# Kernel tuning notes

Hardware: AMD Instinct MI355X
Metric: run time of the kernel (lower is better)

Reference implementation:

```python
import jax, jax.numpy as jnp
import numpy as np

N_DRUG, N_CELL, N_GENE = 1000, 1000, 6000
N = N_DRUG + N_CELL + N_GENE
H1, H2, H3, HEADS = 256, 128, 128, 4
E = 160000
B = 10000


def _gat_layer(x, src, dst, ea, W, b, a_s, a_d, We, a_e, bias, heads, ch):
    # PyG GATConv (single shared lin for src/dst), edge_dim=1, concat=True, slope=0.2
    n = x.shape[0]
    xw = (x @ W + b).reshape(n, heads, ch)                     # [N,H,C]
    a_src = jnp.einsum('nhc,hc->nh', xw, a_s)                  # [N,H]
    a_dst = jnp.einsum('nhc,hc->nh', xw, a_d)
    eemb = (ea[:, None] @ We).reshape(-1, heads, ch)           # [E',H,C]
    a_edge = jnp.einsum('ehc,hc->eh', eemb, a_e)               # [E',H]
    alpha = jax.nn.leaky_relu(a_src[src] + a_dst[dst] + a_edge, 0.2)
    # segment softmax over destination node (flow source->target)
    m = jax.ops.segment_max(alpha, dst, num_segments=n)
    ex = jnp.exp(alpha - m[dst])
    denom = jax.ops.segment_sum(ex, dst, num_segments=n)
    att = ex / (denom[dst] + 1e-16)                            # [E',H]
    out = jax.ops.segment_sum(xw[src] * att[:, :, None], dst, num_segments=n)
    return out.reshape(n, heads * ch) + bias, att


def _graph_norm(x, gamma, beta, mean_scale, eps=1e-5):
    mu = x.mean(0)
    out = x - mean_scale * mu
    var = (out * out).mean(0)
    return gamma * out / jnp.sqrt(var + eps) + beta


def _attn_mat(src, dst, att, n):
    # original sets every edge entry to the scalar mean of all attention weights
    return jnp.zeros((n, n), dtype=att.dtype).at[src, dst].set(att.mean())


def setup_inputs() -> dict:
    key = jax.random.key(0)
    ks = jax.random.split(key, 40)
    s = 0.1
    inp = {
        'drug': jax.random.normal(ks[0], (N_DRUG, N_DRUG), jnp.float32),
        'cell': jax.random.normal(ks[1], (N_CELL, N_CELL), jnp.float32),
        'gene': jax.random.normal(ks[2], (N_GENE, N_GENE), jnp.float32),
        'edge_attr': jax.random.uniform(ks[3], (E,), jnp.float32),
        'edge_index': jax.random.randint(ks[4], (2, E), 0, N),
        'idx_drug': jax.random.randint(ks[5], (B,), 0, N_DRUG),
        'idx_cell': jax.random.randint(ks[6], (B,), 0, N),
        # type-specific input projections
        'W_drug': jax.random.normal(ks[7], (N_DRUG, H1)) * s, 'b_drug': jnp.zeros((H1,)),
        'W_cell': jax.random.normal(ks[8], (N_CELL, H1)) * s, 'b_cell': jnp.zeros((H1,)),
        'W_gene': jax.random.normal(ks[9], (N_GENE, H1)) * s, 'b_gene': jnp.zeros((H1,)),
        # gat1
        'W1': jax.random.normal(ks[10], (H1, HEADS * H2)) * s, 'b1': jnp.zeros((HEADS * H2,)),
        'att_src1': jax.random.normal(ks[11], (HEADS, H2)) * s,
        'att_dst1': jax.random.normal(ks[12], (HEADS, H2)) * s,
        'We1': jax.random.normal(ks[13], (1, HEADS * H2)) * s,
        'att_e1': jax.random.normal(ks[14], (HEADS, H2)) * s,
        'bias1': jnp.zeros((HEADS * H2,)),
        'g1': jnp.ones((HEADS * H2,)), 'be1': jnp.zeros((HEADS * H2,)), 'ms1': jnp.ones((HEADS * H2,)),
        # gat2
        'W2': jax.random.normal(ks[15], (HEADS * H2, HEADS * H3)) * s, 'b2': jnp.zeros((HEADS * H3,)),
        'att_src2': jax.random.normal(ks[16], (HEADS, H3)) * s,
        'att_dst2': jax.random.normal(ks[17], (HEADS, H3)) * s,
        'We2': jax.random.normal(ks[18], (1, HEADS * H3)) * s,
        'att_e2': jax.random.normal(ks[19], (HEADS, H3)) * s,
        'bias2': jnp.zeros((HEADS * H3,)),
        'g2': jnp.ones((HEADS * H3,)), 'be2': jnp.zeros((HEADS * H3,)), 'ms2': jnp.ones((HEADS * H3,)),
        # head
        'Wout': jax.random.normal(ks[20], (2 * HEADS * H3, 1)) * s, 'bout': jnp.zeros((1,)),
    }
    return inp


def reference(drug, cell, gene, edge_attr, edge_index, idx_drug, idx_cell,
              W_drug, b_drug, W_cell, b_cell, W_gene, b_gene,
              W1, b1, att_src1, att_dst1, We1, att_e1, bias1, g1, be1, ms1,
              W2, b2, att_src2, att_dst2, We2, att_e2, bias2, g2, be2, ms2,
              Wout, bout):
    x = jnp.concatenate([drug @ W_drug + b_drug,
                         cell @ W_cell + b_cell,
                         gene @ W_gene + b_gene], axis=0)       # [N,H1]
    # GATConv adds self-loops with edge_attr filled by the mean edge attribute
    loop = jnp.arange(N)
    src = jnp.concatenate([edge_index[0], loop])
    dst = jnp.concatenate([edge_index[1], loop])
    ea = jnp.concatenate([edge_attr, jnp.full((N,), edge_attr.mean(), edge_attr.dtype)])

    x, att1 = _gat_layer(x, src, dst, ea, W1, b1, att_src1, att_dst1, We1, att_e1, bias1, HEADS, H2)
    all_att = _attn_mat(src, dst, att1, N)
    x = jax.nn.relu(_graph_norm(x, g1, be1, ms1))               # dropout = identity (eval)

    x, att2 = _gat_layer(x, src, dst, ea, W2, b2, att_src2, att_dst2, We2, att_e2, bias2, HEADS, H3)
    all_att = all_att + _attn_mat(src, dst, att2, N)
    x = jax.nn.relu(_graph_norm(x, g2, be2, ms2))

    x = jnp.concatenate([x[idx_drug], x[idx_cell]], axis=1) @ Wout + bout  # [B,1]
    return x, all_att
```

## Files before the change

kernel.cpp:

```cpp
#include <hip/hip_runtime.h>
#include <math.h>

#define NDRUG 1000
#define NCELL 1000
#define NGENE 6000
#define NNODE 8000
#define H1 256
#define HD  512
#define E0  160000
#define ET  168000
#define BSZ 10000
#define GKP 6016
#define ZSPLIT 8
#define ZCH 768

typedef __attribute__((ext_vector_type(8))) short bf16x8;
typedef __attribute__((ext_vector_type(4))) float f32x4;

__device__ inline unsigned short f2bf(float f)
{
    unsigned u = __float_as_uint(f);
    u += 0x7fffu + ((u >> 16) & 1u);
    return (unsigned short)(u >> 16);
}
__device__ inline float bf2f(unsigned short h)
{
    return __uint_as_float(((unsigned)h) << 16);
}

__global__ void cvt_pad2_kernel(const float* __restrict__ in,
                                unsigned short* __restrict__ hi,
                                unsigned short* __restrict__ lo,
                                int M, int K, int Mp, int Kp)
{
    long total = (long)Mp * Kp / 8;
    int kp8 = Kp / 8;
    long stride = (long)gridDim.x * blockDim.x;
    for (long u = (long)blockIdx.x * blockDim.x + threadIdx.x; u < total; u += stride) {
        long row = u / kp8; int kc = (int)(u % kp8);
        unsigned short oh[8], ol[8];
        if (row < M && kc * 8 < K) {
            const float* p = in + row * (long)K + kc * 8;
            float4 a = *(const float4*)p, b = *(const float4*)(p + 4);
            float v[8] = {a.x, a.y, a.z, a.w, b.x, b.y, b.z, b.w};
            #pragma unroll
            for (int i = 0; i < 8; ++i) {
                unsigned short h = f2bf(v[i]);
                oh[i] = h;
                ol[i] = f2bf(v[i] - bf2f(h));
            }
        } else {
            #pragma unroll
            for (int i = 0; i < 8; ++i) { oh[i] = 0; ol[i] = 0; }
        }
        *(uint4*)(hi + u * 8) = *(const uint4*)oh;
        *(uint4*)(lo + u * 8) = *(const uint4*)ol;
    }
}

__global__ __launch_bounds__(256) void transpose_cvt2_kernel(const float* __restrict__ W,
                                                             unsigned short* __restrict__ Wh,
                                                             unsigned short* __restrict__ Wl,
                                                             int K, int N, int Kp)
{
    __shared__ float t[32][33];
    int kb = blockIdx.x * 32, nb = blockIdx.y * 32;
    int tx = threadIdx.x & 31, ty = threadIdx.x >> 5;
    #pragma unroll
    for (int i = 0; i < 32; i += 8) {
        int k = kb + ty + i;
        t[ty + i][tx] = (k < K) ? W[(long)k * N + nb + tx] : 0.f;
    }
    __syncthreads();
    #pragma unroll
    for (int i = 0; i < 32; i += 8) {
        int n = nb + ty + i;
        float v = t[tx][ty + i];
        unsigned short h = f2bf(v);
        Wh[(long)n * Kp + kb + tx] = h;
        Wl[(long)n * Kp + kb + tx] = f2bf(v - bf2f(h));
    }
}

template<int OUTBF>
__global__ __launch_bounds__(256) void gemm_mfma2(const unsigned short* __restrict__ Ah,
                                                  const unsigned short* __restrict__ Al,
                                                  const unsigned short* __restrict__ Bh,
                                                  const unsigned short* __restrict__ Bl,
                                                  const float* __restrict__ bias,
                                                  float* __restrict__ Cf,
                                                  unsigned short* __restrict__ Cbh,
                                                  unsigned short* __restrict__ Cbl,
                                                  unsigned short* __restrict__ Cx,
                                                  int M, int Kp, int N)
{
    __shared__ unsigned short AsH[64 * 64];
    __shared__ unsigned short AsL[64 * 64];
    __shared__ unsigned short BsH[64 * 64];
    __shared__ unsigned short BsL[64 * 64];
    char* AsH8 = (char*)AsH; char* AsL8 = (char*)AsL;
    char* BsH8 = (char*)BsH; char* BsL8 = (char*)BsL;
    int tid = threadIdx.x;
    int w = tid >> 6, l = tid & 63;
    int wr = w >> 1, wc = w & 1;
    int g = l >> 4, r16 = l & 15;
    int row0 = blockIdx.y * 64, col0 = blockIdx.x * 64;
    int srow = tid >> 3, skc = tid & 7;
    int B0 = srow * 128 + skc * 16;       int P0 = B0 ^ ((srow & 7) << 4);
    int r1 = srow + 32;                   int B1 = r1 * 128 + skc * 16;
    int P1 = B1 ^ ((r1 & 7) << 4);
    f32x4 acc[2][2] = {};
    for (int k0 = 0; k0 < Kp; k0 += 64) {
        long a0 = (long)(row0 + srow) * Kp + k0 + skc * 8;
        long a1 = (long)(row0 + srow + 32) * Kp + k0 + skc * 8;
        long b0 = (long)(col0 + srow) * Kp + k0 + skc * 8;
        long b1 = (long)(col0 + srow + 32) * Kp + k0 + skc * 8;
        uint4 ah0 = *(const uint4*)(Ah + a0); uint4 ah1 = *(const uint4*)(Ah + a1);
        uint4 al0 = *(const uint4*)(Al + a0); uint4 al1 = *(const uint4*)(Al + a1);
        uint4 bh0 = *(const uint4*)(Bh + b0); uint4 bh1 = *(const uint4*)(Bh + b1);
        uint4 bl0 = *(const uint4*)(Bl + b0); uint4 bl1 = *(const uint4*)(Bl + b1);
        __syncthreads();
        *(uint4*)(AsH8 + P0) = ah0; *(uint4*)(AsH8 + P1) = ah1;
        *(uint4*)(AsL8 + P0) = al0; *(uint4*)(AsL8 + P1) = al1;
        *(uint4*)(BsH8 + P0) = bh0; *(uint4*)(BsH8 + P1) = bh1;
        *(uint4*)(BsL8 + P0) = bl0; *(uint4*)(BsL8 + P1) = bl1;
        __syncthreads();
        #pragma unroll
        for (int kk = 0; kk < 2; ++kk) {
            bf16x8 afh[2], afl[2], bfh[2], bfl[2];
            #pragma unroll
            for (int m = 0; m < 2; ++m) {
                int row = wr * 32 + m * 16 + r16;
                int Bb = (row * 128 + kk * 64 + g * 16) ^ ((row & 7) << 4);
                afh[m] = *(const bf16x8*)(AsH8 + Bb);
                afl[m] = *(const bf16x8*)(AsL8 + Bb);
            }
            #pragma unroll
            for (int n = 0; n < 2; ++n) {
                int row = wc * 32 + n * 16 + r16;
                int Bb = (row * 128 + kk * 64 + g * 16) ^ ((row & 7) << 4);
                bfh[n] = *(const bf16x8*)(BsH8 + Bb);
                bfl[n] = *(const bf16x8*)(BsL8 + Bb);
            }
            #pragma unroll
            for (int m = 0; m < 2; ++m)
                #pragma unroll
                for (int n = 0; n < 2; ++n) {
                    acc[m][n] = __builtin_amdgcn_mfma_f32_16x16x32_bf16(afh[m], bfh[n], acc[m][n], 0, 0, 0);
                    acc[m][n] = __builtin_amdgcn_mfma_f32_16x16x32_bf16(afh[m], bfl[n], acc[m][n], 0, 0, 0);
                    acc[m][n] = __builtin_amdgcn_mfma_f32_16x16x32_bf16(afl[m], bfh[n], acc[m][n], 0, 0, 0);
                }
        }
    }
    #pragma unroll
    for (int m = 0; m < 2; ++m) {
        #pragma unroll
        for (int n = 0; n < 2; ++n) {
            #pragma unroll
            for (int r = 0; r < 4; ++r) {
                int rowg = row0 + wr * 32 + m * 16 + g * 4 + r;
                int colg = col0 + wc * 32 + n * 16 + r16;
                if (rowg < M) {
                    float v = acc[m][n][r] + bias[colg];
                    if (OUTBF) {
                        unsigned short h = f2bf(v);
                        Cbh[(long)rowg * N + colg] = h;
                        Cbl[(long)rowg * N + colg] = f2bf(v - bf2f(h));
                    } else {
                        Cf[(long)rowg * N + colg] = v;
                        Cx[(long)rowg * N + colg] = f2bf(v);
                    }
                }
            }
        }
    }
}

__global__ __launch_bounds__(256) void gemm_gene_f32(const float* __restrict__ A,
                                                     const unsigned short* __restrict__ Bh,
                                                     const unsigned short* __restrict__ Bl,
                                                     float* __restrict__ part)
{
    __shared__ char lds[32768];
    char* AsH = lds;          char* AsL = lds + 8192;
    char* BsH = lds + 16384;  char* BsL = lds + 24576;
    int tid = threadIdx.x;
    int w = tid >> 6, l = tid & 63;
    int wr = w >> 1, wc = w & 1;
    int g = l >> 4, r16 = l & 15;
    int pid = blockIdx.x;
    int L = (pid & 7) * 94 + (pid >> 3);
    int xb = L & 1;
    int yb = (L >> 1) % 47;
    int z  = L / 94;
    int row0 = yb * 128, col0 = xb * 128;
    int kbeg = z * ZCH;
    int kend = kbeg + ZCH; if (kend > GKP) kend = GKP;
    int arow = tid >> 1, akp = (tid & 1) * 16;
    int t_ar = (arow + (arow >> 2)) & 3;
    int s0 = akp >> 3;
    int wb0 = arow * 64 + ((s0 ^ t_ar) << 4);
    int wb1 = arow * 64 + (((s0 + 1) ^ t_ar) << 4);
    int tA = (r16 + (r16 >> 2)) & 3;
    int soA = (g ^ tA) << 4;
    f32x4 acc[4][4] = {};
    for (int k0 = kbeg; k0 < kend; k0 += 32) {
        int gr = row0 + arow;
        int gk = k0 + akp;
        float av[16];
        #pragma unroll
        for (int j = 0; j < 16; j += 4) {
            float4 v = (gr < NGENE && gk + j < NGENE)
                     ? *(const float4*)(A + (long)gr * NGENE + gk + j)
                     : make_float4(0.f, 0.f, 0.f, 0.f);
            av[j] = v.x; av[j + 1] = v.y; av[j + 2] = v.z; av[j + 3] = v.w;
        }
        unsigned short ah[16], alr[16];
        #pragma unroll
        for (int j = 0; j < 16; ++j) {
            ah[j]  = f2bf(av[j]);
            alr[j] = f2bf(av[j] - bf2f(ah[j]));
        }
        const unsigned short* bsh = Bh + (long)(col0 + arow) * GKP + gk;
        const unsigned short* bsl = Bl + (long)(col0 + arow) * GKP + gk;
        uint4 bh0 = *(const uint4*)bsh, bh1 = *(const uint4*)(bsh + 8);
        uint4 bl0 = *(const uint4*)bsl, bl1 = *(const uint4*)(bsl + 8);
        __syncthreads();
        *(uint4*)(AsH + wb0) = *(const uint4*)&ah[0];
        *(uint4*)(AsH + wb1) = *(const uint4*)&ah[8];
        *(uint4*)(AsL + wb0) = *(const uint4*)&alr[0];
        *(uint4*)(AsL + wb1) = *(const uint4*)&alr[8];
        *(uint4*)(BsH + wb0) = bh0; *(uint4*)(BsH + wb1) = bh1;
        *(uint4*)(BsL + wb0) = bl0; *(uint4*)(BsL + wb1) = bl1;
        __syncthreads();
        bf16x8 afh[4], afl[4], bfh[4], bfl[4];
        #pragma unroll
        for (int m = 0; m < 4; ++m) {
            int Bb = (wr * 64 + m * 16 + r16) * 64 + soA;
            afh[m] = *(const bf16x8*)(AsH + Bb);
            afl[m] = *(const bf16x8*)(AsL + Bb);
        }
        #pragma unroll
        for (int n = 0; n < 4; ++n) {
            int Bb = (wc * 64 + n * 16 + r16) * 64 + soA;
            bfh[n] = *(const bf16x8*)(BsH + Bb);
            bfl[n] = *(const bf16x8*)(BsL + Bb);
        }
        #pragma unroll
        for (int m = 0; m < 4; ++m)
            #pragma unroll
            for (int n = 0; n < 4; ++n) {
                acc[m][n] = __builtin_amdgcn_mfma_f32_16x16x32_bf16(afh[m], bfh[n], acc[m][n], 0, 0, 0);
                acc[m][n] = __builtin_amdgcn_mfma_f32_16x16x32_bf16(afh[m], bfl[n], acc[m][n], 0, 0, 0);
                acc[m][n] = __builtin_amdgcn_mfma_f32_16x16x32_bf16(afl[m], bfh[n], acc[m][n], 0, 0, 0);
            }
    }
    #pragma unroll
    for (int m = 0; m < 4; ++m) {
        #pragma unroll
        for (int n = 0; n < 4; ++n) {
            #pragma unroll
            for (int r = 0; r < 4; ++r) {
                int rowg = row0 + wr * 64 + m * 16 + g * 4 + r;
                int colg = col0 + wc * 64 + n * 16 + r16;
                if (rowg < NGENE)
                    part[((long)z * NGENE + rowg) * H1 + colg] = acc[m][n][r];
            }
        }
    }
}

__global__ __launch_bounds__(256) void reduce_splitk_kernel(const float* __restrict__ part,
                                                            const float* __restrict__ bias,
                                                            unsigned short* __restrict__ xh,
                                                            unsigned short* __restrict__ xl)
{
    const long NEL = (long)NGENE * H1;
    long stride = (long)gridDim.x * blockDim.x;
    for (long q = (long)blockIdx.x * blockDim.x + threadIdx.x; q * 4 < NEL; q += stride) {
        long e = q * 4;
        float4 sv = *(const float4*)(part + e);
        #pragma unroll
        for (int z = 1; z < ZSPLIT; ++z) {
            float4 t = *(const float4*)(part + (long)z * NEL + e);
            sv.x += t.x; sv.y += t.y; sv.z += t.z; sv.w += t.w;
        }
        int col = (int)(e & (H1 - 1));
        float4 b = *(const float4*)(bias + col);
        float v[4] = {sv.x + b.x, sv.y + b.y, sv.z + b.z, sv.w + b.w};
        unsigned short oh[4], ol[4];
        #pragma unroll
        for (int i = 0; i < 4; ++i) {
            oh[i] = f2bf(v[i]);
            ol[i] = f2bf(v[i] - bf2f(oh[i]));
        }
        long o = (long)(NDRUG + NCELL) * H1 + e;
        *(uint2*)(xh + o) = *(const uint2*)oh;
        *(uint2*)(xl + o) = *(const uint2*)ol;
    }
}

__global__ void init1_kernel(float* m, int* deg, float* colstats, float* scal)
{
    int i = blockIdx.x * 256 + threadIdx.x;
    if (i < NNODE * 4) m[i] = -3.402823466e38f;
    if (i < NNODE) deg[i] = 0;
    if (i < 1024) colstats[i] = 0.f;
    if (i < 8) scal[i] = 0.f;
}

__global__ void init2_kernel(float* m, float* colstats)
{
    int i = blockIdx.x * 256 + threadIdx.x;
    if (i < NNODE * 4) m[i] = -3.402823466e38f;
    if (i < 1024) colstats[i] = 0.f;
}

__global__ void reduce_sum_kernel(const float* __restrict__ x, int n, float* out)
{
    float s = 0.f;
    for (int i = blockIdx.x * blockDim.x + threadIdx.x; i < n; i += gridDim.x * blockDim.x)
        s += x[i];
    for (int off = 32; off; off >>= 1) s += __shfl_down(s, off);
    if ((threadIdx.x & 63) == 0) atomicAdd(out, s);
}

__global__ __launch_bounds__(512) void ce_kernel(const float* We1, const float* ae1,
                                                 const float* We2, const float* ae2, float* ce)
{
    __shared__ float sm[512];
    int t = threadIdx.x;
    sm[t] = We1[t] * ae1[t];
    __syncthreads();
    if (t < 4) { float s = 0.f; for (int c = 0; c < 128; ++c) s += sm[t * 128 + c]; ce[t] = s; }
    __syncthreads();
    sm[t] = We2[t] * ae2[t];
    __syncthreads();
    if (t < 4) { float s = 0.f; for (int c = 0; c < 128; ++c) s += sm[t * 128 + c]; ce[4 + t] = s; }
}

__global__ void deg_kernel(const int* __restrict__ ei, int* __restrict__ deg)
{
    int e = blockIdx.x * blockDim.x + threadIdx.x;
    if (e >= ET) return;
    int d = (e < E0) ? ei[E0 + e] : (e - E0);
    atomicAdd(&deg[d], 1);
}

__global__ __launch_bounds__(1024) void scan_kernel(const int* __restrict__ deg,
                                                    int* __restrict__ row_start,
                                                    int* __restrict__ cursor)
{
    __shared__ int sm[1024];
    int t = threadIdx.x;
    int base = t * 8;
    int loc[8];
    int sum = 0;
    #pragma unroll
    for (int j = 0; j < 8; ++j) {
        int v = (base + j < NNODE) ? deg[base + j] : 0;
        loc[j] = sum; sum += v;
    }
    sm[t] = sum;
    __syncthreads();
    for (int off = 1; off < 1024; off <<= 1) {
        int v = (t >= off) ? sm[t - off] : 0;
        __syncthreads();
        sm[t] += v;
        __syncthreads();
    }
    int excl = sm[t] - sum;
    #pragma unroll
    for (int j = 0; j < 8; ++j) {
        int idx = base + j;
        if (idx < NNODE) { int v = excl + loc[j]; row_start[idx] = v; cursor[idx] = v; }
    }
    if (t == 1023) row_start[NNODE] = sm[1023];
}

__global__ void scatter_csr_kernel(const int* __restrict__ ei, int* __restrict__ cursor,
                                   int* __restrict__ csr_src, int* __restrict__ pos_of_e)
{
    int e = blockIdx.x * blockDim.x + threadIdx.x;
    if (e >= ET) return;
    int s, d;
    if (e < E0) { s = ei[e]; d = ei[E0 + e]; }
    else        { s = d = e - E0; }
    int pos = atomicAdd(&cursor[d], 1);
    csr_src[pos] = s;
    pos_of_e[e] = pos;
}

__global__ __launch_bounds__(256) void attn_coef_kernel(const float* __restrict__ xw,
                                                        const float* __restrict__ as,
                                                        const float* __restrict__ ad,
                                                        float* __restrict__ a_src,
                                                        float* __restrict__ a_dst)
{
    int n = blockIdx.x * 4 + (threadIdx.x >> 6);
    int l = threadIdx.x & 63;
    #pragma unroll
    for (int h = 0; h < 4; ++h) {
        float x1 = xw[(long)n * HD + h * 128 + l];
        float x2 = xw[(long)n * HD + h * 128 + 64 + l];
        float s = x1 * as[h * 128 + l] + x2 * as[h * 128 + 64 + l];
        float d = x1 * ad[h * 128 + l] + x2 * ad[h * 128 + 64 + l];
        for (int off = 32; off; off >>= 1) { s += __shfl_down(s, off); d += __shfl_down(d, off); }
        if (l == 0) { a_src[n * 4 + h] = s; a_dst[n * 4 + h] = d; }
    }
}

__device__ inline void atomicMaxF(float* addr, float v)
{
    if (v >= 0.f) atomicMax((int*)addr, __float_as_int(v));
    else          atomicMin((unsigned int*)addr, __float_as_uint(v));
}

__global__ void alpha_max_kernel(const int* __restrict__ ei, const float* __restrict__ eattr,
                                 const float* __restrict__ scal,
                                 const float* __restrict__ a_src, const float* __restrict__ a_dst,
                                 const float* __restrict__ ce,
                                 float* __restrict__ csr_alpha,
                                 const int* __restrict__ pos_of_e,
                                 float* __restrict__ m)
{
    int e = blockIdx.x * blockDim.x + threadIdx.x;
    if (e >= ET) return;
    int s, d; float a;
    if (e < E0) { s = ei[e]; d = ei[E0 + e]; a = eattr[e]; }
    else        { s = d = e - E0; a = scal[0] * (1.0f / E0); }
    float4 av;
    float* avp = (float*)&av;
    #pragma unroll
    for (int h = 0; h < 4; ++h) {
        float v = a_src[s * 4 + h] + a_dst[d * 4 + h] + a * ce[h];
        v = v > 0.f ? v : 0.2f * v;
        avp[h] = v;
        atomicMaxF(&m[d * 4 + h], v);
    }
    *(float4*)(csr_alpha + (long)pos_of_e[e] * 4) = av;
}

__global__ __launch_bounds__(256) void aggregate_kernel(const unsigned short* __restrict__ xwb,
                                                        const float* __restrict__ csr_alpha,
                                                        const float* __restrict__ m,
                                                        const int* __restrict__ rs,
                                                        const int* __restrict__ csr_src,
                                                        const float* __restrict__ bias,
                                                        float* __restrict__ out)
{
    int n = blockIdx.x;
    int h = threadIdx.x >> 6;
    int l = threadIdx.x & 63;
    float mnh = m[n * 4 + h];
    int i0 = rs[n], i1 = rs[n + 1];
    float den = 0.f;
    for (int i = i0 + l; i < i1; i += 64)
        den += expf(csr_alpha[(long)i * 4 + h] - mnh);
    for (int off = 32; off; off >>= 1) den += __shfl_down(den, off);
    den = __shfl(den, 0);
    float rden = 1.0f / (den + 1e-16f);
    float acc0 = 0.f, acc1 = 0.f;
    int i = i0;
    for (; i + 7 < i1; i += 8) {
        int      sv[8];
        float    av[8];
        unsigned xv[8];
        #pragma unroll
        for (int j = 0; j < 8; ++j) {
            sv[j] = csr_src[i + j];
            av[j] = csr_alpha[(long)(i + j) * 4 + h];
        }
        #pragma unroll
        for (int j = 0; j < 8; ++j)
            xv[j] = *(const unsigned*)(xwb + (long)sv[j] * HD + h * 128 + 2 * l);
        #pragma unroll
        for (int j = 0; j < 8; ++j) {
            float w = expf(av[j] - mnh);
            acc0 += w * bf2f((unsigned short)(xv[j] & 0xffffu));
            acc1 += w * bf2f((unsigned short)(xv[j] >> 16));
        }
    }
    for (; i < i1; ++i) {
        int s = csr_src[i];
        float w = expf(csr_alpha[(long)i * 4 + h] - mnh);
        unsigned x = *(const unsigned*)(xwb + (long)s * HD + h * 128 + 2 * l);
        acc0 += w * bf2f((unsigned short)(x & 0xffffu));
        acc1 += w * bf2f((unsigned short)(x >> 16));
    }
    float2 o;
    o.x = acc0 * rden + bias[h * 128 + 2 * l];
    o.y = acc1 * rden + bias[h * 128 + 2 * l + 1];
    *(float2*)(out + (long)n * HD + h * 128 + 2 * l) = o;
}

__global__ __launch_bounds__(256) void colstats_kernel(const float* __restrict__ x,
                                                       float* __restrict__ colsum,
                                                       float* __restrict__ colsumsq)
{
    int t = threadIdx.x, b = blockIdx.x;
    float s0 = 0.f, s1 = 0.f, q0 = 0.f, q1 = 0.f;
    for (int r = b * 125; r < (b + 1) * 125; ++r) {
        float v0 = x[(long)r * HD + t];
        float v1 = x[(long)r * HD + t + 256];
        s0 += v0; q0 += v0 * v0;
        s1 += v1; q1 += v1 * v1;
    }
    atomicAdd(&colsum[t], s0);
    atomicAdd(&colsum[t + 256], s1);
    atomicAdd(&colsumsq[t], q0);
    atomicAdd(&colsumsq[t + 256], q1);
}

__global__ void norm_kernel(float* __restrict__ x,
                            unsigned short* __restrict__ xbh, unsigned short* __restrict__ xbl,
                            const float* __restrict__ colsum,
                            const float* __restrict__ colsumsq,
                            const float* __restrict__ g, const float* __restrict__ be,
                            const float* __restrict__ ms)
{
    int stride = gridDim.x * blockDim.x;
    for (int idx = blockIdx.x * blockDim.x + threadIdx.x; idx < NNODE * HD; idx += stride) {
        int j = idx & 511;
        float mu  = colsum[j] * (1.0f / NNODE);
        float ex2 = colsumsq[j] * (1.0f / NNODE);
        float msj = ms[j];
        float var = ex2 - msj * (2.0f - msj) * mu * mu;
        float v = x[idx] - msj * mu;
        float y = g[j] * v / sqrtf(var + 1e-5f) + be[j];
        y = y > 0.f ? y : 0.f;
        x[idx] = y;
        unsigned short h = f2bf(y);
        xbh[idx] = h;
        xbl[idx] = f2bf(y - bf2f(h));
    }
}

__global__ __launch_bounds__(256) void head_kernel(const float* __restrict__ x2,
                                                   const int* __restrict__ idd,
                                                   const int* __restrict__ idc,
                                                   const float* __restrict__ Wout,
                                                   const float* __restrict__ bout,
                                                   float* __restrict__ out0)
{
    int w = threadIdx.x >> 6, l = threadIdx.x & 63;
    int b = blockIdx.x * 4 + w;
    if (b >= BSZ) return;
    int rd = idd[b], rc = idc[b];
    float s = 0.f;
    #pragma unroll
    for (int k = l; k < HD; k += 64)
        s += x2[(long)rd * HD + k] * Wout[k] + x2[(long)rc * HD + k] * Wout[HD + k];
    for (int off = 32; off; off >>= 1) s += __shfl_down(s, off);
    if (l == 0) out0[b] = s + bout[0];
}

__global__ void zero_f4_kernel(float4* __restrict__ p, long n4)
{
    long stride = (long)gridDim.x * blockDim.x;
    for (long i = (long)blockIdx.x * blockDim.x + threadIdx.x; i < n4; i += stride)
        p[i] = make_float4(0.f, 0.f, 0.f, 0.f);
}

__global__ void scatter_att_kernel(const int* __restrict__ ei, float* __restrict__ attm)
{
    int e = blockIdx.x * blockDim.x + threadIdx.x;
    if (e >= ET) return;
    int s, d;
    if (e < E0) { s = ei[e]; d = ei[E0 + e]; }
    else        { s = d = e - E0; }
    const float val = 2.0f * (float)NNODE / (float)ET;
    attm[(long)s * NNODE + d] = val;
}

extern "C" void kernel_launch(void* const* d_in, const int* in_sizes, int n_in,
                              void* d_out, int out_size, void* d_ws, size_t ws_size,
                              hipStream_t stream)
{
    const float* drug   = (const float*)d_in[0];
    const float* cell   = (const float*)d_in[1];
    const float* gene   = (const float*)d_in[2];
    const float* eattr  = (const float*)d_in[3];
    const int*   ei     = (const int*)d_in[4];
    const int*   idd    = (const int*)d_in[5];
    const int*   idc    = (const int*)d_in[6];
    const float* Wdrug  = (const float*)d_in[7];
    const float* bdrug  = (const float*)d_in[8];
    const float* Wcell  = (const float*)d_in[9];
    const float* bcell  = (const float*)d_in[10];
    const float* Wgene  = (const float*)d_in[11];
    const float* bgene  = (const float*)d_in[12];
    const float* W1     = (const float*)d_in[13];
    const float* b1     = (const float*)d_in[14];
    const float* as1    = (const float*)d_in[15];
    const float* ad1    = (const float*)d_in[16];
    const float* We1    = (const float*)d_in[17];
    const float* ae1    = (const float*)d_in[18];
    const float* bias1  = (const float*)d_in[19];
    const float* g1     = (const float*)d_in[20];
    const float* be1    = (const float*)d_in[21];
    const float* ms1    = (const float*)d_in[22];
    const float* W2     = (const float*)d_in[23];
    const float* b2     = (const float*)d_in[24];
    const float* as2    = (const float*)d_in[25];
    const float* ad2    = (const float*)d_in[26];
    const float* We2    = (const float*)d_in[27];
    const float* ae2    = (const float*)d_in[28];
    const float* bias2  = (const float*)d_in[29];
    const float* g2     = (const float*)d_in[30];
    const float* be2    = (const float*)d_in[31];
    const float* ms2    = (const float*)d_in[32];
    const float* Wout   = (const float*)d_in[33];
    const float* bout   = (const float*)d_in[34];

    float* out0 = (float*)d_out;
    float* attm = (float*)d_out + BSZ;

    float* ws     = (float*)d_ws;
    float* xw     = ws;
    float* outb   = xw + (long)NNODE * HD;
    float* csr_al = outb + (long)NNODE * HD;
    float* a_src  = csr_al + (long)ET * 4;
    float* a_dst  = a_src + NNODE * 4;
    float* mbuf   = a_dst + NNODE * 4;
    float* colsum = mbuf + NNODE * 4;
    float* colsq  = colsum + 512;
    float* ce     = colsq + 512;
    float* scal   = ce + 8;
    int* deg      = (int*)(scal + 8);
    int* rs       = deg + NNODE;
    int* cursor   = rs + NNODE + 4;
    int* csr_src  = cursor + NNODE;
    int* pos_of_e = csr_src + ET;
    unsigned short* p = (unsigned short*)(pos_of_e + ET);
    unsigned short* xwb    = p; p += (long)NNODE * HD;
    unsigned short* drug_h = p; p += (long)1024 * 1024;
    unsigned short* drug_l = p; p += (long)1024 * 1024;
    unsigned short* cell_h = p; p += (long)1024 * 1024;
    unsigned short* cell_l = p; p += (long)1024 * 1024;
    unsigned short* x0_h   = p; p += (long)NNODE * H1;
    unsigned short* x0_l   = p; p += (long)NNODE * H1;
    unsigned short* xb_h   = p; p += (long)NNODE * HD;
    unsigned short* xb_l   = p; p += (long)NNODE * HD;
    unsigned short* Wd_h   = p; p += 256 * 1024;
    unsigned short* Wd_l   = p; p += 256 * 1024;
    unsigned short* Wc_h   = p; p += 256 * 1024;
    unsigned short* Wc_l   = p; p += 256 * 1024;
    unsigned short* Wg_h   = p; p += 256 * GKP;
    unsigned short* Wg_l   = p; p += 256 * GKP;
    unsigned short* W1_h   = p; p += 512 * 256;
    unsigned short* W1_l   = p; p += 512 * 256;
    unsigned short* W2_h   = p; p += 512 * 512;
    unsigned short* W2_l   = p; p += 512 * 512;
    float* partsk = (float*)((((unsigned long long)p) + 15) & ~15ULL);

    dim3 blk256(256);
    int gE = (ET + 255) / 256;

    init1_kernel<<<125, blk256, 0, stream>>>(mbuf, deg, colsum, scal);
    deg_kernel<<<gE, blk256, 0, stream>>>(ei, deg);
    scan_kernel<<<1, 1024, 0, stream>>>(deg, rs, cursor);
    scatter_csr_kernel<<<gE, blk256, 0, stream>>>(ei, cursor, csr_src, pos_of_e);
    reduce_sum_kernel<<<64, blk256, 0, stream>>>(eattr, E0, &scal[0]);
    ce_kernel<<<1, 512, 0, stream>>>(We1, ae1, We2, ae2, ce);

    cvt_pad2_kernel<<<512, blk256, 0, stream>>>(drug, drug_h, drug_l, NDRUG, NDRUG, 1024, 1024);
    cvt_pad2_kernel<<<512, blk256, 0, stream>>>(cell, cell_h, cell_l, NCELL, NCELL, 1024, 1024);
    transpose_cvt2_kernel<<<dim3(32, 8),  blk256, 0, stream>>>(Wdrug, Wd_h, Wd_l, NDRUG, H1, 1024);
    transpose_cvt2_kernel<<<dim3(32, 8),  blk256, 0, stream>>>(Wcell, Wc_h, Wc_l, NCELL, H1, 1024);
    transpose_cvt2_kernel<<<dim3(188, 8), blk256, 0, stream>>>(Wgene, Wg_h, Wg_l, NGENE, H1, GKP);
    transpose_cvt2_kernel<<<dim3(8, 16),  blk256, 0, stream>>>(W1, W1_h, W1_l, H1, HD, H1);
    transpose_cvt2_kernel<<<dim3(16, 16), blk256, 0, stream>>>(W2, W2_h, W2_l, HD, HD, HD);

    gemm_mfma2<1><<<dim3(H1 / 64, 16), blk256, 0, stream>>>(drug_h, drug_l, Wd_h, Wd_l, bdrug,
        nullptr, x0_h, x0_l, nullptr, NDRUG, 1024, H1);
    gemm_mfma2<1><<<dim3(H1 / 64, 16), blk256, 0, stream>>>(cell_h, cell_l, Wc_h, Wc_l, bcell,
        nullptr, x0_h + (long)NDRUG * H1, x0_l + (long)NDRUG * H1, nullptr, NCELL, 1024, H1);
    gemm_gene_f32<<<752, blk256, 0, stream>>>(gene, Wg_h, Wg_l, partsk);
    reduce_splitk_kernel<<<1500, blk256, 0, stream>>>(partsk, bgene, x0_h, x0_l);

    gemm_mfma2<0><<<dim3(HD / 64, NNODE / 64), blk256, 0, stream>>>(x0_h, x0_l, W1_h, W1_l, b1,
        xw, nullptr, nullptr, xwb, NNODE, H1, HD);
    attn_coef_kernel<<<NNODE / 4, blk256, 0, stream>>>(xw, as1, ad1, a_src, a_dst);
    alpha_max_kernel<<<gE, blk256, 0, stream>>>(ei, eattr, scal, a_src, a_dst, ce,
        csr_al, pos_of_e, mbuf);
    aggregate_kernel<<<NNODE, blk256, 0, stream>>>(xwb, csr_al, mbuf, rs, csr_src, bias1, outb);
    colstats_kernel<<<64, blk256, 0, stream>>>(outb, colsum, colsq);
    norm_kernel<<<2048, blk256, 0, stream>>>(outb, xb_h, xb_l, colsum, colsq, g1, be1, ms1);

    gemm_mfma2<0><<<dim3(HD / 64, NNODE / 64), blk256, 0, stream>>>(xb_h, xb_l, W2_h, W2_l, b2,
        xw, nullptr, nullptr, xwb, NNODE, HD, HD);
    attn_coef_kernel<<<NNODE / 4, blk256, 0, stream>>>(xw, as2, ad2, a_src, a_dst);
    init2_kernel<<<125, blk256, 0, stream>>>(mbuf, colsum);
    alpha_max_kernel<<<gE, blk256, 0, stream>>>(ei, eattr, scal, a_src, a_dst, ce + 4,
        csr_al, pos_of_e, mbuf);
    aggregate_kernel<<<NNODE, blk256, 0, stream>>>(xwb, csr_al, mbuf, rs, csr_src, bias2, outb);
    colstats_kernel<<<64, blk256, 0, stream>>>(outb, colsum, colsq);
    norm_kernel<<<2048, blk256, 0, stream>>>(outb, xb_h, xb_l, colsum, colsq, g2, be2, ms2);

    head_kernel<<<(BSZ + 3) / 4, blk256, 0, stream>>>(outb, idd, idc, Wout, bout, out0);
    zero_f4_kernel<<<2048, blk256, 0, stream>>>((float4*)attm, (long)NNODE * NNODE / 4);
    scatter_att_kernel<<<gE, blk256, 0, stream>>>(ei, attm);
}
```

Baseline: 580.8 us.

## Double-buffer gene GEMM LDS and batch small preprocessing kernels into fewer launches

The split-K gene GEMM now double-buffers its LDS tiles, prefetching the next K slice into registers while MFMAs run on the current buffer. This drops one barrier per iteration and hides global load latency. The bf16 hi part is now truncation instead of round-to-nearest, with the lo residual still capturing the error. Separately, the two cvt_pad launches, five transpose launches and two small reduction launches are merged into single batched kernels to cut launch overhead. LDS use doubles to 64KB, which may reduce occupancy.

```diff
diff --git a/kernel.cpp b/kernel.cpp
--- a/kernel.cpp
+++ b/kernel.cpp
@@ -28,19 +28,20 @@
     return __uint_as_float(((unsigned)h) << 16);
 }
 
-__global__ void cvt_pad2_kernel(const float* __restrict__ in,
-                                unsigned short* __restrict__ hi,
-                                unsigned short* __restrict__ lo,
-                                int M, int K, int Mp, int Kp)
-{
-    long total = (long)Mp * Kp / 8;
-    int kp8 = Kp / 8;
-    long stride = (long)gridDim.x * blockDim.x;
-    for (long u = (long)blockIdx.x * blockDim.x + threadIdx.x; u < total; u += stride) {
-        long row = u / kp8; int kc = (int)(u % kp8);
+__global__ void cvt_pad2_dc_kernel(const float* __restrict__ drug, unsigned short* dh, unsigned short* dl,
+                                   const float* __restrict__ cell, unsigned short* ch, unsigned short* cl)
+{
+    const float* in;
+    unsigned short *hi, *lo;
+    long u0;
+    if (blockIdx.x < 512) { in = drug; hi = dh; lo = dl; u0 = (long)blockIdx.x * 256 + threadIdx.x; }
+    else                  { in = cell; hi = ch; lo = cl; u0 = (long)(blockIdx.x - 512) * 256 + threadIdx.x; }
+    const long total = (long)1024 * 1024 / 8;
+    for (long u = u0; u < total; u += 512 * 256) {
+        long row = u / 128; int kc = (int)(u % 128);
         unsigned short oh[8], ol[8];
-        if (row < M && kc * 8 < K) {
-            const float* p = in + row * (long)K + kc * 8;
+        if (row < 1000 && kc * 8 < 1000) {
+            const float* p = in + row * 1000 + kc * 8;
             float4 a = *(const float4*)p, b = *(const float4*)(p + 4);
             float v[8] = {a.x, a.y, a.z, a.w, b.x, b.y, b.z, b.w};
             #pragma unroll
@@ -58,13 +59,29 @@
     }
 }
 
-__global__ __launch_bounds__(256) void transpose_cvt2_kernel(const float* __restrict__ W,
-                                                             unsigned short* __restrict__ Wh,
-                                                             unsigned short* __restrict__ Wl,
-                                                             int K, int N, int Kp)
-{
+
+struct TC5 {
+    const float* W[5];
+    unsigned short* Wh[5];
+    unsigned short* Wl[5];
+    int K[5]; int N[5]; int Kp[5]; int gx[5];
+    int start[6];
+};
+
+__global__ __launch_bounds__(256) void transpose_cvt2_batch(TC5 d)
+{
+    int bid = blockIdx.x;
+    int idx = 0;
+    #pragma unroll
+    for (int i = 1; i < 5; ++i) if (bid >= d.start[i]) idx = i;
+    int local = bid - d.start[idx];
+    int gx = d.gx[idx];
+    int K = d.K[idx], N = d.N[idx], Kp = d.Kp[idx];
+    const float* W = d.W[idx];
+    unsigned short* Wh = d.Wh[idx];
+    unsigned short* Wl = d.Wl[idx];
     __shared__ float t[32][33];
-    int kb = blockIdx.x * 32, nb = blockIdx.y * 32;
+    int kb = (local % gx) * 32, nb = (local / gx) * 32;
     int tx = threadIdx.x & 31, ty = threadIdx.x >> 5;
     #pragma unroll
     for (int i = 0; i < 32; i += 8) {
@@ -181,9 +198,7 @@
                                                      const unsigned short* __restrict__ Bl,
                                                      float* __restrict__ part)
 {
-    __shared__ char lds[32768];
-    char* AsH = lds;          char* AsL = lds + 8192;
-    char* BsH = lds + 16384;  char* BsL = lds + 24576;
+    __shared__ char lds[65536];
     int tid = threadIdx.x;
     int w = tid >> 6, l = tid & 63;
     int wr = w >> 1, wc = w & 1;
@@ -196,64 +211,110 @@
     int row0 = yb * 128, col0 = xb * 128;
     int kbeg = z * ZCH;
     int kend = kbeg + ZCH; if (kend > GKP) kend = GKP;
+    int niter = (kend - kbeg) >> 5;
     int arow = tid >> 1, akp = (tid & 1) * 16;
     int t_ar = (arow + (arow >> 2)) & 3;
     int s0 = akp >> 3;
-    int wb0 = arow * 64 + ((s0 ^ t_ar) << 4);
-    int wb1 = arow * 64 + (((s0 + 1) ^ t_ar) << 4);
+    int wo0 = arow * 64 + ((s0 ^ t_ar) << 4);
+    int wo1 = arow * 64 + (((s0 + 1) ^ t_ar) << 4);
     int tA = (r16 + (r16 >> 2)) & 3;
     int soA = (g ^ tA) << 4;
+    int gr = row0 + arow;
+    const float* arowp = A + (long)gr * NGENE;
+    const unsigned short* bhp = Bh + (long)(col0 + arow) * GKP;
+    const unsigned short* blp = Bl + (long)(col0 + arow) * GKP;
+    bool arok = (gr < NGENE);
     f32x4 acc[4][4] = {};
-    for (int k0 = kbeg; k0 < kend; k0 += 32) {
-        int gr = row0 + arow;
-        int gk = k0 + akp;
-        float av[16];
+
+    float av[16];
+    uint4 rbh0, rbh1, rbl0, rbl1;
+    {
+        int gk = kbeg + akp;
         #pragma unroll
         for (int j = 0; j < 16; j += 4) {
-            float4 v = (gr < NGENE && gk + j < NGENE)
-                     ? *(const float4*)(A + (long)gr * NGENE + gk + j)
-                     : make_float4(0.f, 0.f, 0.f, 0.f);
+            float4 v = (arok && gk + j < NGENE) ? *(const float4*)(arowp + gk + j)
+                                                : make_float4(0.f, 0.f, 0.f, 0.f);
             av[j] = v.x; av[j + 1] = v.y; av[j + 2] = v.z; av[j + 3] = v.w;
         }
+        rbh0 = *(const uint4*)(bhp + gk); rbh1 = *(const uint4*)(bhp + gk + 8);
+        rbl0 = *(const uint4*)(blp + gk); rbl1 = *(const uint4*)(blp + gk + 8);
+    }
+    {
         unsigned short ah[16], alr[16];
         #pragma unroll
         for (int j = 0; j < 16; ++j) {
-            ah[j]  = f2bf(av[j]);
-            alr[j] = f2bf(av[j] - bf2f(ah[j]));
-        }
-        const unsigned short* bsh = Bh + (long)(col0 + arow) * GKP + gk;
-        const unsigned short* bsl = Bl + (long)(col0 + arow) * GKP + gk;
-        uint4 bh0 = *(const uint4*)bsh, bh1 = *(const uint4*)(bsh + 8);
-        uint4 bl0 = *(const uint4*)bsl, bl1 = *(const uint4*)(bsl + 8);
+            unsigned u = __float_as_uint(av[j]);
+            ah[j] = (unsigned short)(u >> 16);
+            alr[j] = f2bf(av[j] - __uint_as_float(u & 0xffff0000u));
+        }
+        char* AsH = lds; char* AsL = lds + 8192;
+        char* BsH = lds + 16384; char* BsL = lds + 24576;
+        *(uint4*)(AsH + wo0) = *(const uint4*)&ah[0];
+        *(uint4*)(AsH + wo1) = *(const uint4*)&ah[8];
+        *(uint4*)(AsL + wo0) = *(const uint4*)&alr[0];
+        *(uint4*)(AsL + wo1) = *(const uint4*)&alr[8];
+        *(uint4*)(BsH + wo0) = rbh0; *(uint4*)(BsH + wo1) = rbh1;
+        *(uint4*)(BsL + wo0) = rbl0; *(uint4*)(BsL + wo1) = rbl1;
+    }
+    __syncthreads();
+    for (int i = 0; i < niter; ++i) {
+        bool more = (i + 1 < niter);
+        if (more) {
+            int gk = kbeg + (i + 1) * 32 + akp;
+            #pragma unroll
+            for (int j = 0; j < 16; j += 4) {
+                float4 v = (arok && gk + j < NGENE) ? *(const float4*)(arowp + gk + j)
+                                                    : make_float4(0.f, 0.f, 0.f, 0.f);
+                av[j] = v.x; av[j + 1] = v.y; av[j + 2] = v.z; av[j + 3] = v.w;
+            }
+            rbh0 = *(const uint4*)(bhp + gk); rbh1 = *(const uint4*)(bhp + gk + 8);
+            rbl0 = *(const uint4*)(blp + gk); rbl1 = *(const uint4*)(blp + gk + 8);
+        }
+        {
+            char* base = lds + (i & 1) * 32768;
+            char* AsH = base; char* AsL = base + 8192;
+            char* BsH = base + 16384; char* BsL = base + 24576;
+            bf16x8 afh[4], afl[4], bfh[4], bfl[4];
+            #pragma unroll
+            for (int m = 0; m < 4; ++m) {
+                int Bb = (wr * 64 + m * 16 + r16) * 64 + soA;
+                afh[m] = *(const bf16x8*)(AsH + Bb);
+                afl[m] = *(const bf16x8*)(AsL + Bb);
+            }
+            #pragma unroll
+            for (int n = 0; n < 4; ++n) {
+                int Bb = (wc * 64 + n * 16 + r16) * 64 + soA;
+                bfh[n] = *(const bf16x8*)(BsH + Bb);
+                bfl[n] = *(const bf16x8*)(BsL + Bb);
+            }
+            #pragma unroll
+            for (int m = 0; m < 4; ++m)
+                #pragma unroll
+                for (int n = 0; n < 4; ++n) {
+                    acc[m][n] = __builtin_amdgcn_mfma_f32_16x16x32_bf16(afh[m], bfh[n], acc[m][n], 0, 0, 0);
+                    acc[m][n] = __builtin_amdgcn_mfma_f32_16x16x32_bf16(afh[m], bfl[n], acc[m][n], 0, 0, 0);
+                    acc[m][n] = __builtin_amdgcn_mfma_f32_16x16x32_bf16(afl[m], bfh[n], acc[m][n], 0, 0, 0);
+                }
+        }
+        if (more) {
+            unsigned short ah[16], alr[16];
+            #pragma unroll
+            for (int j = 0; j < 16; ++j) {
+                unsigned u = __float_as_uint(av[j]);
+                ah[j] = (unsigned short)(u >> 16);
+                alr[j] = f2bf(av[j] - __uint_as_float(u & 0xffff0000u));
+            }
+            char* base = lds + ((i + 1) & 1) * 32768;
+            char* AsH = base; char* AsL = base + 8192;
+            char* BsH = base + 16384; char* BsL = base + 24576;
+            *(uint4*)(AsH + wo0) = *(const uint4*)&ah[0];
+            *(uint4*)(AsH + wo1) = *(const uint4*)&ah[8];
+            *(uint4*)(AsL + wo0) = *(const uint4*)&alr[0];
+            *(uint4*)(AsL + wo1) = *(const uint4*)&alr[8];
+            *(uint4*)(BsH + wo0) = rbh0; *(uint4*)(BsH + wo1) = rbh1;
+            *(uint4*)(BsL + wo0) = rbl0; *(uint4*)(BsL + wo1) = rbl1;
+        }
         __syncthreads();
-        *(uint4*)(AsH + wb0) = *(const uint4*)&ah[0];
-        *(uint4*)(AsH + wb1) = *(const uint4*)&ah[8];
-        *(uint4*)(AsL + wb0) = *(const uint4*)&alr[0];
-        *(uint4*)(AsL + wb1) = *(const uint4*)&alr[8];
-        *(uint4*)(BsH + wb0) = bh0; *(uint4*)(BsH + wb1) = bh1;
-        *(uint4*)(BsL + wb0) = bl0; *(uint4*)(BsL + wb1) = bl1;
-        __syncthreads();
-        bf16x8 afh[4], afl[4], bfh[4], bfl[4];
-        #pragma unroll
-        for (int m = 0; m < 4; ++m) {
-            int Bb = (wr * 64 + m * 16 + r16) * 64 + soA;
-            afh[m] = *(const bf16x8*)(AsH + Bb);
-            afl[m] = *(const bf16x8*)(AsL + Bb);
-        }
-        #pragma unroll
-        for (int n = 0; n < 4; ++n) {
-            int Bb = (wc * 64 + n * 16 + r16) * 64 + soA;
-            bfh[n] = *(const bf16x8*)(BsH + Bb);
-            bfl[n] = *(const bf16x8*)(BsL + Bb);
-        }
-        #pragma unroll
-        for (int m = 0; m < 4; ++m)
-            #pragma unroll
-            for (int n = 0; n < 4; ++n) {
-                acc[m][n] = __builtin_amdgcn_mfma_f32_16x16x32_bf16(afh[m], bfh[n], acc[m][n], 0, 0, 0);
-                acc[m][n] = __builtin_amdgcn_mfma_f32_16x16x32_bf16(afh[m], bfl[n], acc[m][n], 0, 0, 0);
-                acc[m][n] = __builtin_amdgcn_mfma_f32_16x16x32_bf16(afl[m], bfh[n], acc[m][n], 0, 0, 0);
-            }
     }
     #pragma unroll
     for (int m = 0; m < 4; ++m) {
@@ -316,27 +377,27 @@
     if (i < 1024) colstats[i] = 0.f;
 }
 
-__global__ void reduce_sum_kernel(const float* __restrict__ x, int n, float* out)
-{
-    float s = 0.f;
-    for (int i = blockIdx.x * blockDim.x + threadIdx.x; i < n; i += gridDim.x * blockDim.x)
-        s += x[i];
-    for (int off = 32; off; off >>= 1) s += __shfl_down(s, off);
-    if ((threadIdx.x & 63) == 0) atomicAdd(out, s);
-}
-
-__global__ __launch_bounds__(512) void ce_kernel(const float* We1, const float* ae1,
-                                                 const float* We2, const float* ae2, float* ce)
-{
-    __shared__ float sm[512];
-    int t = threadIdx.x;
-    sm[t] = We1[t] * ae1[t];
-    __syncthreads();
-    if (t < 4) { float s = 0.f; for (int c = 0; c < 128; ++c) s += sm[t * 128 + c]; ce[t] = s; }
-    __syncthreads();
-    sm[t] = We2[t] * ae2[t];
-    __syncthreads();
-    if (t < 4) { float s = 0.f; for (int c = 0; c < 128; ++c) s += sm[t * 128 + c]; ce[4 + t] = s; }
+__global__ __launch_bounds__(512) void small_pre_kernel(const float* __restrict__ eattr, float* scal,
+                                                        const float* We1, const float* ae1,
+                                                        const float* We2, const float* ae2, float* ce)
+{
+    if (blockIdx.x < 64) {
+        float s = 0.f;
+        for (int i = blockIdx.x * 512 + threadIdx.x; i < E0; i += 64 * 512)
+            s += eattr[i];
+        for (int off = 32; off; off >>= 1) s += __shfl_down(s, off);
+        if ((threadIdx.x & 63) == 0) atomicAdd(&scal[0], s);
+    } else {
+        __shared__ float sm[512];
+        int t = threadIdx.x;
+        sm[t] = We1[t] * ae1[t];
+        __syncthreads();
+        if (t < 4) { float s = 0.f; for (int c = 0; c < 128; ++c) s += sm[t * 128 + c]; ce[t] = s; }
+        __syncthreads();
+        sm[t] = We2[t] * ae2[t];
+        __syncthreads();
+        if (t < 4) { float s = 0.f; for (int c = 0; c < 128; ++c) s += sm[t * 128 + c]; ce[4 + t] = s; }
+    }
 }
 
 __global__ void deg_kernel(const int* __restrict__ ei, int* __restrict__ deg)
@@ -661,16 +722,20 @@
     deg_kernel<<<gE, blk256, 0, stream>>>(ei, deg);
     scan_kernel<<<1, 1024, 0, stream>>>(deg, rs, cursor);
     scatter_csr_kernel<<<gE, blk256, 0, stream>>>(ei, cursor, csr_src, pos_of_e);
-    reduce_sum_kernel<<<64, blk256, 0, stream>>>(eattr, E0, &scal[0]);
-    ce_kernel<<<1, 512, 0, stream>>>(We1, ae1, We2, ae2, ce);
-
-    cvt_pad2_kernel<<<512, blk256, 0, stream>>>(drug, drug_h, drug_l, NDRUG, NDRUG, 1024, 1024);
-    cvt_pad2_kernel<<<512, blk256, 0, stream>>>(cell, cell_h, cell_l, NCELL, NCELL, 1024, 1024);
-    transpose_cvt2_kernel<<<dim3(32, 8),  blk256, 0, stream>>>(Wdrug, Wd_h, Wd_l, NDRUG, H1, 1024);
-    transpose_cvt2_kernel<<<dim3(32, 8),  blk256, 0, stream>>>(Wcell, Wc_h, Wc_l, NCELL, H1, 1024);
-    transpose_cvt2_kernel<<<dim3(188, 8), blk256, 0, stream>>>(Wgene, Wg_h, Wg_l, NGENE, H1, GKP);
-    transpose_cvt2_kernel<<<dim3(8, 16),  blk256, 0, stream>>>(W1, W1_h, W1_l, H1, HD, H1);
-    transpose_cvt2_kernel<<<dim3(16, 16), blk256, 0, stream>>>(W2, W2_h, W2_l, HD, HD, HD);
+    small_pre_kernel<<<65, 512, 0, stream>>>(eattr, scal, We1, ae1, We2, ae2, ce);
+
+    cvt_pad2_dc_kernel<<<1024, blk256, 0, stream>>>(drug, drug_h, drug_l, cell, cell_h, cell_l);
+    {
+        TC5 d;
+        d.W[0] = Wdrug; d.Wh[0] = Wd_h; d.Wl[0] = Wd_l; d.K[0] = NDRUG; d.N[0] = H1; d.Kp[0] = 1024; d.gx[0] = 32;
+        d.W[1] = Wcell; d.Wh[1] = Wc_h; d.Wl[1] = Wc_l; d.K[1] = NCELL; d.N[1] = H1; d.Kp[1] = 1024; d.gx[1] = 32;
+        d.W[2] = Wgene; d.Wh[2] = Wg_h; d.Wl[2] = Wg_l; d.K[2] = NGENE; d.N[2] = H1; d.Kp[2] = GKP;  d.gx[2] = 188;
+        d.W[3] = W1;    d.Wh[3] = W1_h; d.Wl[3] = W1_l; d.K[3] = H1;    d.N[3] = HD; d.Kp[3] = H1;   d.gx[3] = 8;
+        d.W[4] = W2;    d.Wh[4] = W2_h; d.Wl[4] = W2_l; d.K[4] = HD;    d.N[4] = HD; d.Kp[4] = HD;   d.gx[4] = 16;
+        d.start[0] = 0;    d.start[1] = 256;  d.start[2] = 512;
+        d.start[3] = 2016; d.start[4] = 2144; d.start[5] = 2400;
+        transpose_cvt2_batch<<<2400, blk256, 0, stream>>>(d);
+    }
 
     gemm_mfma2<1><<<dim3(H1 / 64, 16), blk256, 0, stream>>>(drug_h, drug_l, Wd_h, Wd_l, bdrug,
         nullptr, x0_h, x0_l, nullptr, NDRUG, 1024, H1);
```

After: 576.2 us. About the same (-0.8%).
